# Kernel optimization log

Hardware: AMD Instinct MI355X
Metric: run time of the kernel (lower is better)

The kernel has to match this reference:

```python
import jax, jax.numpy as jnp
import numpy as np

T, N, F_IN, H, C, E = 64, 2000, 32, 64, 10, 32000
EPS = 1e-5  # BatchNorm eps (PyG BatchNorm default)


def setup_inputs() -> dict:
    key = jax.random.key(0)
    ks = jax.random.split(key, 32)
    nrm = lambda i, shape, s=0.05: jax.random.normal(ks[i], shape, jnp.float32) * s
    return {
        "x_seq": jax.random.normal(ks[0], (T, N, F_IN), jnp.float32),
        "edge_index": jax.random.randint(ks[1], (2, E), 0, N),
        "edge_weight": jax.random.uniform(ks[2], (E,), jnp.float32),
        "causal_weight": nrm(3, (N, N), 0.01),  # torch.randn(N,N)*0.01
        "lin_in_w": nrm(4, (H, F_IN)), "lin_in_b": nrm(5, (H,)),
        "fusion_w": nrm(6, (H, 2 * H)), "fusion_b": nrm(7, (H,)),
        "gcn_w0": nrm(8, (H, H)), "gcn_b0": nrm(9, (H,)),
        "gcn_w1": nrm(10, (H, H)), "gcn_b1": nrm(11, (H,)),
        "bn0_g": jnp.ones((H,), jnp.float32), "bn0_b": jnp.zeros((H,), jnp.float32),
        "bn0_m": nrm(12, (H,)), "bn0_v": 0.5 + jax.random.uniform(ks[13], (H,), jnp.float32),
        "bn1_g": jnp.ones((H,), jnp.float32), "bn1_b": jnp.zeros((H,), jnp.float32),
        "bn1_m": nrm(14, (H,)), "bn1_v": 0.5 + jax.random.uniform(ks[15], (H,), jnp.float32),
        "gru_wih0": nrm(16, (3 * H, H)), "gru_whh0": nrm(17, (3 * H, H)),
        "gru_bih0": nrm(18, (3 * H,)), "gru_bhh0": nrm(19, (3 * H,)),
        "gru_wih1": nrm(20, (3 * H, H)), "gru_whh1": nrm(21, (3 * H, H)),
        "gru_bih1": nrm(22, (3 * H,)), "gru_bhh1": nrm(23, (3 * H,)),
        "bnout_g": jnp.ones((H,), jnp.float32), "bnout_b": jnp.zeros((H,), jnp.float32),
        "bnout_m": nrm(24, (H,)), "bnout_v": 0.5 + jax.random.uniform(ks[25], (H,), jnp.float32),
        "lin_out_w": nrm(26, (C, H)), "lin_out_b": nrm(27, (C,)),
    }


def _bn(x, g, b, m, v):
    # eval-mode BatchNorm over the feature (last) axis with running stats
    return (x - m) * jax.lax.rsqrt(v + EPS) * g + b


def _gru_layer(xs, wih, whh, bih, bhh):
    # torch nn.GRU single layer, batch_first=False: xs [T, B, H_in]
    n_batch, h = xs.shape[1], whh.shape[1]

    def step(hprev, xt):
        gi = xt @ wih.T + bih            # [B, 3H]
        gh = hprev @ whh.T + bhh         # [B, 3H]
        i_r, i_z, i_n = jnp.split(gi, 3, axis=-1)
        h_r, h_z, h_n = jnp.split(gh, 3, axis=-1)
        r = jax.nn.sigmoid(i_r + h_r)
        z = jax.nn.sigmoid(i_z + h_z)
        n = jnp.tanh(i_n + r * h_n)
        hnew = (1.0 - z) * n + z * hprev
        return hnew, hnew

    h0 = jnp.zeros((n_batch, h), xs.dtype)
    _, ys = jax.lax.scan(step, h0, xs)
    return ys


def reference(x_seq, edge_index, edge_weight, causal_weight, lin_in_w, lin_in_b,
              fusion_w, fusion_b, gcn_w0, gcn_b0, gcn_w1, gcn_b1,
              bn0_g, bn0_b, bn0_m, bn0_v, bn1_g, bn1_b, bn1_m, bn1_v,
              gru_wih0, gru_whh0, gru_bih0, gru_bhh0,
              gru_wih1, gru_whh1, gru_bih1, gru_bhh1,
              bnout_g, bnout_b, bnout_m, bnout_v, lin_out_w, lin_out_b):
    n = x_seq.shape[1]
    src, dst = edge_index[0], edge_index[1]
    loops = jnp.arange(n)
    # GCN normalization with added self-loops (PyG gcn_norm, fill_value=1)
    src_f = jnp.concatenate([src, loops])
    dst_f = jnp.concatenate([dst, loops])
    w_f = jnp.concatenate([edge_weight, jnp.ones((n,), edge_weight.dtype)])
    deg = jnp.zeros((n,), x_seq.dtype).at[dst_f].add(w_f)
    dis = jax.lax.rsqrt(jnp.maximum(deg, 1e-12))
    norm = dis[src_f] * w_f * dis[dst_f]             # [E+N]

    # per-timestep pipeline, vectorized over T (same math as the Python loop)
    x = jax.nn.relu(jnp.einsum('tnf,hf->tnh', x_seq, lin_in_w) + lin_in_b)  # [T,N,H]
    wc = jax.nn.softmax(causal_weight, axis=1)                              # [N,N]
    x_agg = jnp.einsum('ij,tjh->tih', wc, x)
    x = jax.nn.relu(jnp.concatenate([x, x_agg], axis=-1) @ fusion_w.T + fusion_b)

    def gcn(xx, w, b):
        xw = xx @ w.T                                         # [T,N,H]
        msgs = jnp.take(xw, src_f, axis=1) * norm[None, :, None]  # [T,E+N,H]
        agg = jnp.zeros_like(xw).at[:, dst_f].add(msgs)
        return agg + b

    x = jax.nn.relu(_bn(gcn(x, gcn_w0, gcn_b0), bn0_g, bn0_b, bn0_m, bn0_v))
    # dropout between GCN layers is identity in eval mode
    x = jax.nn.relu(_bn(gcn(x, gcn_w1, gcn_b1), bn1_g, bn1_b, bn1_m, bn1_v))

    h = _gru_layer(x, gru_wih0, gru_whh0, gru_bih0, gru_bhh0)
    h = _gru_layer(h, gru_wih1, gru_whh1, gru_bih1, gru_bhh1)
    h_last = jax.nn.relu(_bn(h[-1], bnout_g, bnout_b, bnout_m, bnout_v))
    out = h_last @ lin_out_w.T + lin_out_b                   # [N, C]
    return jax.nn.log_softmax(out, axis=-1)
```

## Files before the change

### kernel.cpp

```cpp
#include <hip/hip_runtime.h>
#include <hip/hip_bf16.h>
#include <math.h>

#define TT 64
#define NN 2000
#define FIN 32
#define HH 64
#define CC 10
#define EE 32000
#define ETOT 34000
#define THL 4096
#define EPSBN 1e-5f
#define NB 16

#define OFF_WC   0u
#define OFF_XA   4000000u
#define OFF_XB   12192000u
#define OFF_XC   20384000u
#define OFF_DEG  28576000u
#define OFF_H1   28578048u
#define OFF_CNT  28706048u
#define OFF_CUR  28708096u
#define OFF_OFF  28710144u
#define OFF_CSRS 28712208u
#define OFF_CSRN 28746224u
#define OFF_HST  28780240u

typedef __attribute__((ext_vector_type(8))) short short8v;
typedef __attribute__((ext_vector_type(4))) float f32x4;

__device__ __forceinline__ float fsigmoid(float x) { return 1.f / (1.f + __expf(-x)); }
__device__ __forceinline__ float ftanh(float x) {
    float e = __expf(2.f * x);
    return (e - 1.f) / (e + 1.f);
}
__device__ __forceinline__ unsigned short f2bf(float f) {
    __hip_bfloat16 h = __float2bfloat16(f);
    return *reinterpret_cast<unsigned short*>(&h);
}
__device__ __forceinline__ float bf2f(unsigned short u) {
    unsigned int x = ((unsigned int)u) << 16;
    return __int_as_float(x);
}
__device__ __forceinline__ void gload_lds16(const unsigned short* g, unsigned short* l) {
    __builtin_amdgcn_global_load_lds(
        (const __attribute__((address_space(1))) unsigned int*)g,
        (__attribute__((address_space(3))) unsigned int*)l,
        16, 0, 0);
}

__global__ void k_zero(int* cnt, int* cur, float* deg) {
    int i = blockIdx.x * 256 + threadIdx.x;
    if (i < 2048) { cnt[i] = 0; cur[i] = 0; deg[i] = 0.f; }
}

__global__ void k_count(const int* __restrict__ ei, const float* __restrict__ ew,
                        int* cnt, float* deg) {
    int e = blockIdx.x * 256 + threadIdx.x;
    if (e < ETOT) {
        int dst; float w;
        if (e < EE) { dst = ei[EE + e]; w = ew[e]; }
        else        { dst = e - EE;     w = 1.f; }
        atomicAdd(&cnt[dst], 1);
        atomicAdd(&deg[dst], w);
    }
}

__global__ __launch_bounds__(1024) void k_scan(const int* __restrict__ cnt, int* off) {
    __shared__ int s[2048];
    int tid = threadIdx.x;
    s[tid]        = (tid        < NN) ? cnt[tid]        : 0;
    s[tid + 1024] = (tid + 1024 < NN) ? cnt[tid + 1024] : 0;
    __syncthreads();
    for (int d = 1; d < 2048; d <<= 1) {
        int idx = (tid + 1) * (d << 1) - 1;
        if (idx < 2048) s[idx] += s[idx - d];
        __syncthreads();
    }
    if (tid == 0) s[2047] = 0;
    __syncthreads();
    for (int d = 1024; d >= 1; d >>= 1) {
        int idx = (tid + 1) * (d << 1) - 1;
        if (idx < 2048) { int t = s[idx - d]; s[idx - d] = s[idx]; s[idx] += t; }
        __syncthreads();
    }
    off[tid] = s[tid];
    off[tid + 1024] = s[tid + 1024];
}

__global__ void k_fill(const int* __restrict__ ei, const float* __restrict__ ew,
                       const float* __restrict__ deg, const int* __restrict__ off,
                       int* cur, int* csr_src, float* csr_nrm) {
    int e = blockIdx.x * 256 + threadIdx.x;
    if (e < ETOT) {
        int src, dst; float w;
        if (e < EE) { src = ei[e]; dst = ei[EE + e]; w = ew[e]; }
        else        { src = dst = e - EE;            w = 1.f; }
        float ds = rsqrtf(fmaxf(deg[src], 1e-12f));
        float dd = rsqrtf(fmaxf(deg[dst], 1e-12f));
        int pos = off[dst] + atomicAdd(&cur[dst], 1);
        csr_src[pos] = src;
        csr_nrm[pos] = ds * w * dd;
    }
}

__global__ __launch_bounds__(256) void k_softmax(const float* __restrict__ CW,
                                                 unsigned short* __restrict__ WCH) {
    __shared__ float row[NN];
    __shared__ float red[256];
    int r = blockIdx.x, tid = threadIdx.x;
    const float* in = CW + (size_t)r * NN;
    float mx = -1e30f;
    for (int i = tid; i < NN; i += 256) { float v = in[i]; row[i] = v; mx = fmaxf(mx, v); }
    red[tid] = mx; __syncthreads();
    for (int s = 128; s > 0; s >>= 1) {
        if (tid < s) red[tid] = fmaxf(red[tid], red[tid + s]);
        __syncthreads();
    }
    mx = red[0]; __syncthreads();
    float sm = 0.f;
    for (int i = tid; i < NN; i += 256) { float e = __expf(row[i] - mx); row[i] = e; sm += e; }
    red[tid] = sm; __syncthreads();
    for (int s = 128; s > 0; s >>= 1) {
        if (tid < s) red[tid] += red[tid + s];
        __syncthreads();
    }
    float inv = 1.f / red[0];
    unsigned short* out = WCH + (size_t)r * 2048;
    for (int i = tid; i < 2048; i += 256)
        out[i] = (i < NN) ? f2bf(row[i] * inv) : (unsigned short)0;
}

__global__ __launch_bounds__(256) void k_lin2(const float* __restrict__ XS,
                                              const float* __restrict__ W,
                                              const float* __restrict__ b,
                                              float* __restrict__ OUT) {
    __shared__ float Wt[FIN][68];
    __shared__ float As[FIN][68];
    int tid = threadIdx.x;
    int n = blockIdx.x;
    for (int i = tid; i < HH * FIN; i += 256) { int o = i >> 5, k = i & 31; Wt[k][o] = W[i]; }
    int row = tid >> 2, kq = tid & 3;
    {
        const float4* src = (const float4*)(XS + ((size_t)row * NN + n) * FIN + kq * 8);
        float4 v0 = src[0], v1 = src[1];
        As[kq * 8 + 0][row] = v0.x; As[kq * 8 + 1][row] = v0.y;
        As[kq * 8 + 2][row] = v0.z; As[kq * 8 + 3][row] = v0.w;
        As[kq * 8 + 4][row] = v1.x; As[kq * 8 + 5][row] = v1.y;
        As[kq * 8 + 6][row] = v1.z; As[kq * 8 + 7][row] = v1.w;
    }
    __syncthreads();
    int tx = tid & 15, ty = tid >> 4;
    float acc[4][4] = {};
#pragma unroll
    for (int k = 0; k < FIN; ++k) {
        float4 av = *(const float4*)&As[k][ty * 4];
        float4 wv = *(const float4*)&Wt[k][tx * 4];
        acc[0][0] += av.x * wv.x; acc[0][1] += av.x * wv.y; acc[0][2] += av.x * wv.z; acc[0][3] += av.x * wv.w;
        acc[1][0] += av.y * wv.x; acc[1][1] += av.y * wv.y; acc[1][2] += av.y * wv.z; acc[1][3] += av.y * wv.w;
        acc[2][0] += av.z * wv.x; acc[2][1] += av.z * wv.y; acc[2][2] += av.z * wv.z; acc[2][3] += av.z * wv.w;
        acc[3][0] += av.w * wv.x; acc[3][1] += av.w * wv.y; acc[3][2] += av.w * wv.z; acc[3][3] += av.w * wv.w;
    }
    float4 bv = *(const float4*)(b + tx * 4);
#pragma unroll
    for (int ii = 0; ii < 4; ++ii) {
        float4 o;
        o.x = fmaxf(acc[ii][0] + bv.x, 0.f);
        o.y = fmaxf(acc[ii][1] + bv.y, 0.f);
        o.z = fmaxf(acc[ii][2] + bv.z, 0.f);
        o.w = fmaxf(acc[ii][3] + bv.w, 0.f);
        *(float4*)(OUT + ((size_t)n * TT + ty * 4 + ii) * HH + tx * 4) = o;
    }
}

__global__ __launch_bounds__(256) void k_tr(const float* __restrict__ X,
                                            unsigned short* __restrict__ XT) {
    __shared__ unsigned short tile[64][65];
    int cb = blockIdx.x * 64;
    int kb = blockIdx.y * 64;
    int tid = threadIdx.x;
    int r = tid >> 2, cq = tid & 3;
    const float4* src = (const float4*)(X + (size_t)(kb + r) * THL + cb + cq * 16);
#pragma unroll
    for (int j = 0; j < 4; ++j) {
        float4 v = src[j];
        tile[cq * 16 + j * 4 + 0][r] = f2bf(v.x);
        tile[cq * 16 + j * 4 + 1][r] = f2bf(v.y);
        tile[cq * 16 + j * 4 + 2][r] = f2bf(v.z);
        tile[cq * 16 + j * 4 + 3][r] = f2bf(v.w);
    }
    __syncthreads();
    int cl = tid >> 2, kq = tid & 3;
    unsigned short tmp[16];
#pragma unroll
    for (int j = 0; j < 16; ++j) tmp[j] = tile[cl][kq * 16 + j];
    unsigned short* dst = XT + (size_t)(cb + cl) * 2048 + kb + kq * 16;
    *(uint4*)dst = *(uint4*)tmp;
    *(uint4*)(dst + 8) = *(uint4*)(tmp + 8);
}

__global__ __launch_bounds__(256, 1) void k_gemm_bf(const unsigned short* __restrict__ A,
                                                    const unsigned short* __restrict__ B,
                                                    unsigned short* __restrict__ CH) {
    __shared__ unsigned short As[128][64];
    __shared__ unsigned short Bs[128][64];
    int tid = threadIdx.x;
    int mb = blockIdx.y * 128, nb = blockIdx.x * 128;
    int w = tid >> 6, lane = tid & 63;
    int wr = w >> 1, wc = w & 1;
    int l15 = lane & 15, l4 = lane >> 4;
    f32x4 acc[4][4] = {};
    int r_base = w * 8 + (lane >> 3);
    int colu = (lane & 7) * 8;
    for (int kt = 0; kt < 32; ++kt) {
        __syncthreads();
#pragma unroll
        for (int c = 0; c < 4; ++c) {
            int row = c * 32 + r_base;
            gload_lds16(A + (size_t)(mb + row) * 2048 + kt * 64 + colu, &As[c * 32 + w * 8][0]);
            gload_lds16(B + (size_t)(nb + row) * 2048 + kt * 64 + colu, &Bs[c * 32 + w * 8][0]);
        }
        __syncthreads();
#pragma unroll
        for (int kk = 0; kk < 2; ++kk) {
            short8v af[4], bfr[4];
#pragma unroll
            for (int f = 0; f < 4; ++f) {
                af[f]  = *(const short8v*)&As[wr * 64 + f * 16 + l15][kk * 32 + l4 * 8];
                bfr[f] = *(const short8v*)&Bs[wc * 64 + f * 16 + l15][kk * 32 + l4 * 8];
            }
#pragma unroll
            for (int fm = 0; fm < 4; ++fm)
#pragma unroll
                for (int fn = 0; fn < 4; ++fn)
                    acc[fm][fn] = __builtin_amdgcn_mfma_f32_16x16x32_bf16(af[fm], bfr[fn], acc[fm][fn], 0, 0, 0);
        }
    }
    unsigned short* epi = (unsigned short*)(&As[0][0]) + (size_t)w * (16 * 72);
    int erow8 = lane >> 3;
    int ecol8 = lane & 7;
#pragma unroll
    for (int fm = 0; fm < 4; ++fm) {
        __syncthreads();
#pragma unroll
        for (int fn = 0; fn < 4; ++fn)
#pragma unroll
            for (int rr = 0; rr < 4; ++rr)
                epi[(l4 * 4 + rr) * 72 + fn * 16 + l15] = f2bf(acc[fm][fn][rr]);
        __syncthreads();
#pragma unroll
        for (int rh = 0; rh < 2; ++rh) {
            int lrow = rh * 8 + erow8;
            int grow = mb + wr * 64 + fm * 16 + lrow;
            if (grow < NN) {
                *(uint4*)(CH + (size_t)grow * THL + nb + wc * 64 + ecol8 * 8)
                    = *(const uint4*)&epi[lrow * 72 + ecol8 * 8];
            }
        }
    }
}

__global__ __launch_bounds__(256) void k_fus2(const float* __restrict__ X,
                                              const unsigned short* __restrict__ XAH,
                                              const float* __restrict__ W,
                                              const float* __restrict__ b,
                                              float* __restrict__ OUT) {
    __shared__ float Wt[2 * HH][68];
    __shared__ float As[HH][68];
    int tid = threadIdx.x;
    size_t r0 = (size_t)blockIdx.x * 64;
    for (int i = tid; i < HH * 2 * HH; i += 256) { int o = i >> 7, k = i & 127; Wt[k][o] = W[i]; }
    int row = tid >> 2, kq = tid & 3;
    int tx = tid & 15, ty = tid >> 4;
    float acc[4][4] = {};
    __syncthreads();
    {
        const float4* src = (const float4*)(X + (r0 + row) * HH + kq * 16);
#pragma unroll
        for (int j = 0; j < 4; ++j) {
            float4 v = src[j];
            As[kq * 16 + j * 4 + 0][row] = v.x;
            As[kq * 16 + j * 4 + 1][row] = v.y;
            As[kq * 16 + j * 4 + 2][row] = v.z;
            As[kq * 16 + j * 4 + 3][row] = v.w;
        }
    }
    __syncthreads();
#pragma unroll
    for (int k = 0; k < HH; ++k) {
        float4 av = *(const float4*)&As[k][ty * 4];
        float4 wv = *(const float4*)&Wt[k][tx * 4];
        acc[0][0] += av.x * wv.x; acc[0][1] += av.x * wv.y; acc[0][2] += av.x * wv.z; acc[0][3] += av.x * wv.w;
        acc[1][0] += av.y * wv.x; acc[1][1] += av.y * wv.y; acc[1][2] += av.y * wv.z; acc[1][3] += av.y * wv.w;
        acc[2][0] += av.z * wv.x; acc[2][1] += av.z * wv.y; acc[2][2] += av.z * wv.z; acc[2][3] += av.z * wv.w;
        acc[3][0] += av.w * wv.x; acc[3][1] += av.w * wv.y; acc[3][2] += av.w * wv.z; acc[3][3] += av.w * wv.w;
    }
    __syncthreads();
    {
        const uint4* s = (const uint4*)(XAH + (r0 + row) * HH + kq * 16);
        uint4 u0 = s[0], u1 = s[1];
        unsigned short us[16];
        *(uint4*)us = u0; *(uint4*)(us + 8) = u1;
#pragma unroll
        for (int j = 0; j < 16; ++j)
            As[kq * 16 + j][row] = bf2f(us[j]);
    }
    __syncthreads();
#pragma unroll
    for (int k = 0; k < HH; ++k) {
        float4 av = *(const float4*)&As[k][ty * 4];
        float4 wv = *(const float4*)&Wt[HH + k][tx * 4];
        acc[0][0] += av.x * wv.x; acc[0][1] += av.x * wv.y; acc[0][2] += av.x * wv.z; acc[0][3] += av.x * wv.w;
        acc[1][0] += av.y * wv.x; acc[1][1] += av.y * wv.y; acc[1][2] += av.y * wv.z; acc[1][3] += av.y * wv.w;
        acc[2][0] += av.z * wv.x; acc[2][1] += av.z * wv.y; acc[2][2] += av.z * wv.z; acc[2][3] += av.z * wv.w;
        acc[3][0] += av.w * wv.x; acc[3][1] += av.w * wv.y; acc[3][2] += av.w * wv.z; acc[3][3] += av.w * wv.w;
    }
    float4 bv = *(const float4*)(b + tx * 4);
#pragma unroll
    for (int ii = 0; ii < 4; ++ii) {
        float4 o;
        o.x = fmaxf(acc[ii][0] + bv.x, 0.f);
        o.y = fmaxf(acc[ii][1] + bv.y, 0.f);
        o.z = fmaxf(acc[ii][2] + bv.z, 0.f);
        o.w = fmaxf(acc[ii][3] + bv.w, 0.f);
        *(float4*)(OUT + (r0 + ty * 4 + ii) * HH + tx * 4) = o;
    }
}

__global__ __launch_bounds__(256) void k_xw2(const float* __restrict__ IN,
                                             const float* __restrict__ W,
                                             unsigned short* __restrict__ OUT) {
    __shared__ float Wt[HH][68];
    __shared__ float As[HH][68];
    int tid = threadIdx.x;
    size_t r0 = (size_t)blockIdx.x * 64;
    for (int i = tid; i < HH * HH; i += 256) { int o = i >> 6, k = i & 63; Wt[k][o] = W[i]; }
    int row = tid >> 2, kq = tid & 3;
    {
        const float4* src = (const float4*)(IN + (r0 + row) * HH + kq * 16);
#pragma unroll
        for (int j = 0; j < 4; ++j) {
            float4 v = src[j];
            As[kq * 16 + j * 4 + 0][row] = v.x;
            As[kq * 16 + j * 4 + 1][row] = v.y;
            As[kq * 16 + j * 4 + 2][row] = v.z;
            As[kq * 16 + j * 4 + 3][row] = v.w;
        }
    }
    __syncthreads();
    int tx = tid & 15, ty = tid >> 4;
    float acc[4][4] = {};
#pragma unroll
    for (int k = 0; k < HH; ++k) {
        float4 av = *(const float4*)&As[k][ty * 4];
        float4 wv = *(const float4*)&Wt[k][tx * 4];
        acc[0][0] += av.x * wv.x; acc[0][1] += av.x * wv.y; acc[0][2] += av.x * wv.z; acc[0][3] += av.x * wv.w;
        acc[1][0] += av.y * wv.x; acc[1][1] += av.y * wv.y; acc[1][2] += av.y * wv.z; acc[1][3] += av.y * wv.w;
        acc[2][0] += av.z * wv.x; acc[2][1] += av.z * wv.y; acc[2][2] += av.z * wv.z; acc[2][3] += av.z * wv.w;
        acc[3][0] += av.w * wv.x; acc[3][1] += av.w * wv.y; acc[3][2] += av.w * wv.z; acc[3][3] += av.w * wv.w;
    }
#pragma unroll
    for (int ii = 0; ii < 4; ++ii) {
        unsigned int p0 = (unsigned int)f2bf(acc[ii][0]) | ((unsigned int)f2bf(acc[ii][1]) << 16);
        unsigned int p1 = (unsigned int)f2bf(acc[ii][2]) | ((unsigned int)f2bf(acc[ii][3]) << 16);
        uint2 pk; pk.x = p0; pk.y = p1;
        *(uint2*)(OUT + (r0 + ty * 4 + ii) * HH + tx * 4) = pk;
    }
}

__global__ __launch_bounds__(256) void k_agg(const unsigned short* __restrict__ XW,
                                             const int* __restrict__ off,
                                             const int* __restrict__ csr_src,
                                             const float* __restrict__ csr_nrm,
                                             const float* __restrict__ bias,
                                             const float* __restrict__ g,
                                             const float* __restrict__ bb,
                                             const float* __restrict__ m,
                                             const float* __restrict__ v,
                                             float* __restrict__ OUT) {
    int dst = blockIdx.x, ch = blockIdx.y, tid = threadIdx.x;
    int base = ch * 1024 + tid * 4;
    float4 acc = make_float4(0.f, 0.f, 0.f, 0.f);
    int beg = off[dst], end = off[dst + 1];
    for (int e = beg; e < end; ++e) {
        int src = csr_src[e];
        float w = csr_nrm[e];
        uint2 u = *(const uint2*)(XW + (size_t)src * THL + base);
        acc.x += w * bf2f((unsigned short)(u.x & 0xffff));
        acc.y += w * bf2f((unsigned short)(u.x >> 16));
        acc.z += w * bf2f((unsigned short)(u.y & 0xffff));
        acc.w += w * bf2f((unsigned short)(u.y >> 16));
    }
    int h0 = base & 63;
    float4 bs = *(const float4*)(bias + h0);
    float4 gv = *(const float4*)(g + h0);
    float4 vv = *(const float4*)(v + h0);
    float4 mv = *(const float4*)(m + h0);
    float4 bv = *(const float4*)(bb + h0);
    float4 o;
    o.x = fmaxf((acc.x + bs.x - mv.x) * rsqrtf(vv.x + EPSBN) * gv.x + bv.x, 0.f);
    o.y = fmaxf((acc.y + bs.y - mv.y) * rsqrtf(vv.y + EPSBN) * gv.y + bv.y, 0.f);
    o.z = fmaxf((acc.z + bs.z - mv.z) * rsqrtf(vv.z + EPSBN) * gv.z + bv.z, 0.f);
    o.w = fmaxf((acc.w + bs.w - mv.w) * rsqrtf(vv.w + EPSBN) * gv.w + bv.w, 0.f);
    *(float4*)(OUT + (size_t)dst * THL + base) = o;
}

__global__ __launch_bounds__(256, 1) void k_gruM(const float* __restrict__ IN,
                                                 const float* __restrict__ wih0, const float* __restrict__ whh0,
                                                 const float* __restrict__ bih0, const float* __restrict__ bhh0,
                                                 const float* __restrict__ wih1, const float* __restrict__ whh1,
                                                 const float* __restrict__ bih1, const float* __restrict__ bhh1,
                                                 float* __restrict__ hout) {
    __shared__ float hf0[NB][68];
    __shared__ float hf1[NB][68];
    __shared__ unsigned short hb0[NB][72];
    __shared__ unsigned short hb1[NB][72];
    int tid = threadIdx.x;
    int w = tid >> 6, lane = tid & 63;
    int l15 = lane & 15, l4 = lane >> 4;
    int nb0 = blockIdx.x * NB;
    short8v bw[4][3][2];
    const float* Wm[4] = { wih0, whh0, wih1, whh1 };
#pragma unroll
    for (int m = 0; m < 4; ++m)
#pragma unroll
        for (int g = 0; g < 3; ++g)
#pragma unroll
            for (int kk = 0; kk < 2; ++kk) {
                const float* src = Wm[m] + (size_t)(64 * g + 16 * w + l15) * HH + kk * 32 + l4 * 8;
                float4 v0 = *(const float4*)src;
                float4 v1 = *(const float4*)(src + 4);
                short8v f;
                f[0] = (short)f2bf(v0.x); f[1] = (short)f2bf(v0.y);
                f[2] = (short)f2bf(v0.z); f[3] = (short)f2bf(v0.w);
                f[4] = (short)f2bf(v1.x); f[5] = (short)f2bf(v1.y);
                f[6] = (short)f2bf(v1.z); f[7] = (short)f2bf(v1.w);
                bw[m][g][kk] = f;
            }
    int jr = 16 * w + l15;
    float b0r = bih0[jr] + bhh0[jr];
    float b0z = bih0[64 + jr] + bhh0[64 + jr];
    float b0n = bih0[128 + jr];
    float h0n = bhh0[128 + jr];
    float b1r = bih1[jr] + bhh1[jr];
    float b1z = bih1[64 + jr] + bhh1[64 + jr];
    float b1n = bih1[128 + jr];
    float h1n = bhh1[128 + jr];
    for (int i = tid; i < NB * 68; i += 256) { ((float*)hf0)[i] = 0.f; ((float*)hf1)[i] = 0.f; }
    for (int i = tid; i < NB * 72; i += 256) { ((unsigned short*)hb0)[i] = 0; ((unsigned short*)hb1)[i] = 0; }
    __syncthreads();
    const float* xb = IN + (size_t)(nb0 + l15) * (TT * HH);
    float4 xv[4];
    {
        const float* xs = xb + 0 * HH + l4 * 8;
        xv[0] = *(const float4*)xs; xv[1] = *(const float4*)(xs + 4);
        const float* xs2 = xb + 0 * HH + 32 + l4 * 8;
        xv[2] = *(const float4*)xs2; xv[3] = *(const float4*)(xs2 + 4);
    }
#pragma unroll 1
    for (int t = 0; t <= TT; ++t) {
        bool act0 = (t < TT);
        bool act1 = (t >= 1);
        short8v ax[2], ah0[2], ah1[2];
#pragma unroll
        for (int kk = 0; kk < 2; ++kk) {
            float4 v0 = xv[kk * 2], v1 = xv[kk * 2 + 1];
            short8v f;
            f[0] = (short)f2bf(v0.x); f[1] = (short)f2bf(v0.y);
            f[2] = (short)f2bf(v0.z); f[3] = (short)f2bf(v0.w);
            f[4] = (short)f2bf(v1.x); f[5] = (short)f2bf(v1.y);
            f[6] = (short)f2bf(v1.z); f[7] = (short)f2bf(v1.w);
            ax[kk] = f;
            ah0[kk] = *(const short8v*)&hb0[l15][kk * 32 + l4 * 8];
            ah1[kk] = *(const short8v*)&hb1[l15][kk * 32 + l4 * 8];
        }
        __syncthreads();
        if (t + 1 < TT) {
            const float* xs = xb + (size_t)(t + 1) * HH + l4 * 8;
            xv[0] = *(const float4*)xs; xv[1] = *(const float4*)(xs + 4);
            const float* xs2 = xb + (size_t)(t + 1) * HH + 32 + l4 * 8;
            xv[2] = *(const float4*)xs2; xv[3] = *(const float4*)(xs2 + 4);
        }
        if (act0) {
            f32x4 gr = { b0r, b0r, b0r, b0r };
            f32x4 gz = { b0z, b0z, b0z, b0z };
            f32x4 gn = { b0n, b0n, b0n, b0n };
            f32x4 hr = { 0.f, 0.f, 0.f, 0.f };
            f32x4 hz = { 0.f, 0.f, 0.f, 0.f };
            f32x4 hn = { h0n, h0n, h0n, h0n };
#pragma unroll
            for (int kk = 0; kk < 2; ++kk) {
                gr = __builtin_amdgcn_mfma_f32_16x16x32_bf16(ax[kk], bw[0][0][kk], gr, 0, 0, 0);
                gz = __builtin_amdgcn_mfma_f32_16x16x32_bf16(ax[kk], bw[0][1][kk], gz, 0, 0, 0);
                gn = __builtin_amdgcn_mfma_f32_16x16x32_bf16(ax[kk], bw[0][2][kk], gn, 0, 0, 0);
                hr = __builtin_amdgcn_mfma_f32_16x16x32_bf16(ah0[kk], bw[1][0][kk], hr, 0, 0, 0);
                hz = __builtin_amdgcn_mfma_f32_16x16x32_bf16(ah0[kk], bw[1][1][kk], hz, 0, 0, 0);
                hn = __builtin_amdgcn_mfma_f32_16x16x32_bf16(ah0[kk], bw[1][2][kk], hn, 0, 0, 0);
            }
#pragma unroll
            for (int i = 0; i < 4; ++i) {
                int node = l4 * 4 + i;
                float r = fsigmoid(gr[i] + hr[i]);
                float z = fsigmoid(gz[i] + hz[i]);
                float nn2 = ftanh(gn[i] + r * hn[i]);
                float ho = hf0[node][jr];
                float hv = (1.f - z) * nn2 + z * ho;
                hf0[node][jr] = hv;
                hb0[node][jr] = f2bf(hv);
            }
        }
        if (act1) {
            f32x4 gr = { b1r, b1r, b1r, b1r };
            f32x4 gz = { b1z, b1z, b1z, b1z };
            f32x4 gn = { b1n, b1n, b1n, b1n };
            f32x4 hr = { 0.f, 0.f, 0.f, 0.f };
            f32x4 hz = { 0.f, 0.f, 0.f, 0.f };
            f32x4 hn = { h1n, h1n, h1n, h1n };
#pragma unroll
            for (int kk = 0; kk < 2; ++kk) {
                gr = __builtin_amdgcn_mfma_f32_16x16x32_bf16(ah0[kk], bw[2][0][kk], gr, 0, 0, 0);
                gz = __builtin_amdgcn_mfma_f32_16x16x32_bf16(ah0[kk], bw[2][1][kk], gz, 0, 0, 0);
                gn = __builtin_amdgcn_mfma_f32_16x16x32_bf16(ah0[kk], bw[2][2][kk], gn, 0, 0, 0);
                hr = __builtin_amdgcn_mfma_f32_16x16x32_bf16(ah1[kk], bw[3][0][kk], hr, 0, 0, 0);
                hz = __builtin_amdgcn_mfma_f32_16x16x32_bf16(ah1[kk], bw[3][1][kk], hz, 0, 0, 0);
                hn = __builtin_amdgcn_mfma_f32_16x16x32_bf16(ah1[kk], bw[3][2][kk], hn, 0, 0, 0);
            }
#pragma unroll
            for (int i = 0; i < 4; ++i) {
                int node = l4 * 4 + i;
                float r = fsigmoid(gr[i] + hr[i]);
                float z = fsigmoid(gz[i] + hz[i]);
                float nn2 = ftanh(gn[i] + r * hn[i]);
                float ho = hf1[node][jr];
                float hv = (1.f - z) * nn2 + z * ho;
                hf1[node][jr] = hv;
                hb1[node][jr] = f2bf(hv);
            }
        }
        __syncthreads();
    }
    for (int i = tid; i < NB * HH; i += 256) {
        int node = i >> 6, j = i & 63;
        hout[(size_t)(nb0 + node) * HH + j] = hf1[node][j];
    }
}

__global__ __launch_bounds__(256) void k_head(const float* __restrict__ Hf,
                                              const float* __restrict__ g, const float* __restrict__ b,
                                              const float* __restrict__ m, const float* __restrict__ v,
                                              const float* __restrict__ W, const float* __restrict__ wb,
                                              float* __restrict__ out) {
    __shared__ float hb[4][HH];
    __shared__ float lg[4][CC];
    int tid = threadIdx.x;
    int n0 = blockIdx.x * 4;
    int wv = tid >> 6, lane = tid & 63;
    int n = n0 + wv;
    float x = Hf[(size_t)n * HH + lane];
    x = (x - m[lane]) * rsqrtf(v[lane] + EPSBN) * g[lane] + b[lane];
    hb[wv][lane] = fmaxf(x, 0.f);
    __syncthreads();
    if (tid < 4 * CC) {
        int nn = tid / CC, c = tid % CC;
        float acc = wb[c];
        for (int f = 0; f < HH; ++f) acc += hb[nn][f] * W[c * HH + f];
        lg[nn][c] = acc;
    }
    __syncthreads();
    if (tid < 4 * CC) {
        int nn = tid / CC, c = tid % CC;
        float mx = -1e30f;
#pragma unroll
        for (int i = 0; i < CC; ++i) mx = fmaxf(mx, lg[nn][i]);
        float s = 0.f;
#pragma unroll
        for (int i = 0; i < CC; ++i) s += __expf(lg[nn][i] - mx);
        out[(size_t)(n0 + nn) * CC + c] = lg[nn][c] - mx - __logf(s);
    }
}

extern "C" void kernel_launch(void* const* d_in, const int* in_sizes, int n_in,
                              void* d_out, int out_size, void* d_ws, size_t ws_size,
                              hipStream_t stream) {
    const float* x_seq     = (const float*)d_in[0];
    const int*   edge_idx  = (const int*)d_in[1];
    const float* edge_w    = (const float*)d_in[2];
    const float* causal_w  = (const float*)d_in[3];
    const float* lin_in_w  = (const float*)d_in[4];
    const float* lin_in_b  = (const float*)d_in[5];
    const float* fusion_w  = (const float*)d_in[6];
    const float* fusion_b  = (const float*)d_in[7];
    const float* gcn_w0    = (const float*)d_in[8];
    const float* gcn_b0    = (const float*)d_in[9];
    const float* gcn_w1    = (const float*)d_in[10];
    const float* gcn_b1    = (const float*)d_in[11];
    const float* bn0_g = (const float*)d_in[12], *bn0_b = (const float*)d_in[13];
    const float* bn0_m = (const float*)d_in[14], *bn0_v = (const float*)d_in[15];
    const float* bn1_g = (const float*)d_in[16], *bn1_b = (const float*)d_in[17];
    const float* bn1_m = (const float*)d_in[18], *bn1_v = (const float*)d_in[19];
    const float* wih0 = (const float*)d_in[20], *whh0 = (const float*)d_in[21];
    const float* bih0 = (const float*)d_in[22], *bhh0 = (const float*)d_in[23];
    const float* wih1 = (const float*)d_in[24], *whh1 = (const float*)d_in[25];
    const float* bih1 = (const float*)d_in[26], *bhh1 = (const float*)d_in[27];
    const float* bno_g = (const float*)d_in[28], *bno_b = (const float*)d_in[29];
    const float* bno_m = (const float*)d_in[30], *bno_v = (const float*)d_in[31];
    const float* lout_w = (const float*)d_in[32], *lout_b = (const float*)d_in[33];
    float* out = (float*)d_out;

    float* wsf = (float*)d_ws;
    unsigned short* WCH = (unsigned short*)(wsf + OFF_WC);
    float* XA  = wsf + OFF_XA;
    float* XB  = wsf + OFF_XB;
    float* XC  = wsf + OFF_XC;
    unsigned short* XAT = (unsigned short*)(wsf + OFF_XC);
    unsigned short* XBH = (unsigned short*)(wsf + OFF_XB);
    float* DEG = wsf + OFF_DEG;
    int* CNT   = (int*)(wsf + OFF_CNT);
    int* CUR   = (int*)(wsf + OFF_CUR);
    int* OFFP  = (int*)(wsf + OFF_OFF);
    int* CSRS  = (int*)(wsf + OFF_CSRS);
    float* CSRN = wsf + OFF_CSRN;
    float* HST  = wsf + OFF_HST;

    k_zero<<<8, 256, 0, stream>>>(CNT, CUR, DEG);
    k_count<<<(ETOT + 255) / 256, 256, 0, stream>>>(edge_idx, edge_w, CNT, DEG);
    k_scan<<<1, 1024, 0, stream>>>(CNT, OFFP);
    k_fill<<<(ETOT + 255) / 256, 256, 0, stream>>>(edge_idx, edge_w, DEG, OFFP, CUR, CSRS, CSRN);

    hipMemsetAsync(WCH, 0, (size_t)2048 * 2048 * 2, stream);
    k_softmax<<<NN, 256, 0, stream>>>(causal_w, WCH);
    k_lin2<<<NN, 256, 0, stream>>>(x_seq, lin_in_w, lin_in_b, XA);
    dim3 tg(THL / 64, 2048 / 64);
    k_tr<<<tg, 256, 0, stream>>>(XA, XAT);
    dim3 gg(THL / 128, 2048 / 128);
    k_gemm_bf<<<gg, 256, 0, stream>>>(WCH, XAT, XBH);
    k_fus2<<<NN, 256, 0, stream>>>(XA, XBH, fusion_w, fusion_b, XC);
    k_xw2<<<NN, 256, 0, stream>>>(XC, gcn_w0, XBH);
    dim3 ag(NN, 4);
    k_agg<<<ag, 256, 0, stream>>>(XBH, OFFP, CSRS, CSRN, gcn_b0, bn0_g, bn0_b, bn0_m, bn0_v, XA);
    k_xw2<<<NN, 256, 0, stream>>>(XA, gcn_w1, XBH);
    k_agg<<<ag, 256, 0, stream>>>(XBH, OFFP, CSRS, CSRN, gcn_b1, bn1_g, bn1_b, bn1_m, bn1_v, XC);

    k_gruM<<<NN / NB, 256, 0, stream>>>(XC, wih0, whh0, bih0, bhh0,
                                        wih1, whh1, bih1, bhh1, HST);

    k_head<<<NN / 4, 256, 0, stream>>>(HST, bno_g, bno_b, bno_m, bno_v, lout_w, lout_b, out);
}
```

Measured before the change: 362.0 us.

## Fuse GCN weight projections into fusion-linear and first aggregation kernels

The fusion-linear kernel now keeps its ReLU output in shared memory and multiplies it by gcn_w0 in the same block, writing bf16 XW directly. The first aggregation kernel applies bias, BatchNorm and ReLU, then multiplies each block's 16 rows by gcn_w1 in shared memory to produce the second layer's XW. This removes two kernel launches and two fp32 intermediate round trips through global memory. In exchange, every aggregation block reloads the 64x64 weight matrix, and the fusion kernel writes its output in place over its own input rows.

```diff
diff --git a/kernel.cpp b/kernel.cpp
--- a/kernel.cpp
+++ b/kernel.cpp
@@ -260,11 +260,12 @@
     }
 }
 
-__global__ __launch_bounds__(256) void k_fus2(const float* __restrict__ X,
-                                              const unsigned short* __restrict__ XAH,
-                                              const float* __restrict__ W,
-                                              const float* __restrict__ b,
-                                              float* __restrict__ OUT) {
+__global__ __launch_bounds__(256) void k_fusxw(const float* __restrict__ X,
+                                               const unsigned short* __restrict__ XAH,
+                                               const float* __restrict__ W,
+                                               const float* __restrict__ b,
+                                               const float* __restrict__ W0,
+                                               unsigned short* __restrict__ OUT) {
     __shared__ float Wt[2 * HH][68];
     __shared__ float As[HH][68];
     int tid = threadIdx.x;
@@ -316,56 +317,87 @@
         acc[3][0] += av.w * wv.x; acc[3][1] += av.w * wv.y; acc[3][2] += av.w * wv.z; acc[3][3] += av.w * wv.w;
     }
     float4 bv = *(const float4*)(b + tx * 4);
+    __syncthreads();
 #pragma unroll
     for (int ii = 0; ii < 4; ++ii) {
-        float4 o;
-        o.x = fmaxf(acc[ii][0] + bv.x, 0.f);
-        o.y = fmaxf(acc[ii][1] + bv.y, 0.f);
-        o.z = fmaxf(acc[ii][2] + bv.z, 0.f);
-        o.w = fmaxf(acc[ii][3] + bv.w, 0.f);
-        *(float4*)(OUT + (r0 + ty * 4 + ii) * HH + tx * 4) = o;
-    }
-}
-
-__global__ __launch_bounds__(256) void k_xw2(const float* __restrict__ IN,
-                                             const float* __restrict__ W,
-                                             unsigned short* __restrict__ OUT) {
-    __shared__ float Wt[HH][68];
-    __shared__ float As[HH][68];
-    int tid = threadIdx.x;
-    size_t r0 = (size_t)blockIdx.x * 64;
-    for (int i = tid; i < HH * HH; i += 256) { int o = i >> 6, k = i & 63; Wt[k][o] = W[i]; }
-    int row = tid >> 2, kq = tid & 3;
-    {
-        const float4* src = (const float4*)(IN + (r0 + row) * HH + kq * 16);
-#pragma unroll
-        for (int j = 0; j < 4; ++j) {
-            float4 v = src[j];
-            As[kq * 16 + j * 4 + 0][row] = v.x;
-            As[kq * 16 + j * 4 + 1][row] = v.y;
-            As[kq * 16 + j * 4 + 2][row] = v.z;
-            As[kq * 16 + j * 4 + 3][row] = v.w;
-        }
-    }
-    __syncthreads();
-    int tx = tid & 15, ty = tid >> 4;
-    float acc[4][4] = {};
+        As[tx * 4 + 0][ty * 4 + ii] = fmaxf(acc[ii][0] + bv.x, 0.f);
+        As[tx * 4 + 1][ty * 4 + ii] = fmaxf(acc[ii][1] + bv.y, 0.f);
+        As[tx * 4 + 2][ty * 4 + ii] = fmaxf(acc[ii][2] + bv.z, 0.f);
+        As[tx * 4 + 3][ty * 4 + ii] = fmaxf(acc[ii][3] + bv.w, 0.f);
+    }
+    for (int i = tid; i < HH * HH; i += 256) { int o = i >> 6, k = i & 63; Wt[k][o] = W0[i]; }
+    __syncthreads();
+    float a2[4][4] = {};
 #pragma unroll
     for (int k = 0; k < HH; ++k) {
         float4 av = *(const float4*)&As[k][ty * 4];
         float4 wv = *(const float4*)&Wt[k][tx * 4];
-        acc[0][0] += av.x * wv.x; acc[0][1] += av.x * wv.y; acc[0][2] += av.x * wv.z; acc[0][3] += av.x * wv.w;
-        acc[1][0] += av.y * wv.x; acc[1][1] += av.y * wv.y; acc[1][2] += av.y * wv.z; acc[1][3] += av.y * wv.w;
-        acc[2][0] += av.z * wv.x; acc[2][1] += av.z * wv.y; acc[2][2] += av.z * wv.z; acc[2][3] += av.z * wv.w;
-        acc[3][0] += av.w * wv.x; acc[3][1] += av.w * wv.y; acc[3][2] += av.w * wv.z; acc[3][3] += av.w * wv.w;
+        a2[0][0] += av.x * wv.x; a2[0][1] += av.x * wv.y; a2[0][2] += av.x * wv.z; a2[0][3] += av.x * wv.w;
+        a2[1][0] += av.y * wv.x; a2[1][1] += av.y * wv.y; a2[1][2] += av.y * wv.z; a2[1][3] += av.y * wv.w;
+        a2[2][0] += av.z * wv.x; a2[2][1] += av.z * wv.y; a2[2][2] += av.z * wv.z; a2[2][3] += av.z * wv.w;
+        a2[3][0] += av.w * wv.x; a2[3][1] += av.w * wv.y; a2[3][2] += av.w * wv.z; a2[3][3] += av.w * wv.w;
     }
 #pragma unroll
     for (int ii = 0; ii < 4; ++ii) {
-        unsigned int p0 = (unsigned int)f2bf(acc[ii][0]) | ((unsigned int)f2bf(acc[ii][1]) << 16);
-        unsigned int p1 = (unsigned int)f2bf(acc[ii][2]) | ((unsigned int)f2bf(acc[ii][3]) << 16);
+        unsigned int p0 = (unsigned int)f2bf(a2[ii][0]) | ((unsigned int)f2bf(a2[ii][1]) << 16);
+        unsigned int p1 = (unsigned int)f2bf(a2[ii][2]) | ((unsigned int)f2bf(a2[ii][3]) << 16);
         uint2 pk; pk.x = p0; pk.y = p1;
         *(uint2*)(OUT + (r0 + ty * 4 + ii) * HH + tx * 4) = pk;
     }
+}
+
+__global__ __launch_bounds__(256) void k_aggxw(const unsigned short* __restrict__ XW,
+                                               const int* __restrict__ off,
+                                               const int* __restrict__ csr_src,
+                                               const float* __restrict__ csr_nrm,
+                                               const float* __restrict__ bias,
+                                               const float* __restrict__ g,
+                                               const float* __restrict__ bb,
+                                               const float* __restrict__ m,
+                                               const float* __restrict__ v,
+                                               const float* __restrict__ W1,
+                                               unsigned short* __restrict__ OUT) {
+    __shared__ float Rs[HH][18];
+    __shared__ float Wt[HH][68];
+    int dst = blockIdx.x, ch = blockIdx.y, tid = threadIdx.x;
+    int base = ch * 1024 + tid * 4;
+    for (int i = tid; i < HH * HH; i += 256) { int o = i >> 6, k = i & 63; Wt[k][o] = W1[i]; }
+    float4 acc = make_float4(0.f, 0.f, 0.f, 0.f);
+    int beg = off[dst], end = off[dst + 1];
+    for (int e = beg; e < end; ++e) {
+        int src = csr_src[e];
+        float w = csr_nrm[e];
+        uint2 u = *(const uint2*)(XW + (size_t)src * THL + base);
+        acc.x += w * bf2f((unsigned short)(u.x & 0xffff));
+        acc.y += w * bf2f((unsigned short)(u.x >> 16));
+        acc.z += w * bf2f((unsigned short)(u.y & 0xffff));
+        acc.w += w * bf2f((unsigned short)(u.y >> 16));
+    }
+    int h0 = base & 63;
+    int rloc = tid >> 4;
+    float4 bs = *(const float4*)(bias + h0);
+    float4 gv = *(const float4*)(g + h0);
+    float4 vv = *(const float4*)(v + h0);
+    float4 mv = *(const float4*)(m + h0);
+    float4 bv = *(const float4*)(bb + h0);
+    Rs[h0 + 0][rloc] = fmaxf((acc.x + bs.x - mv.x) * rsqrtf(vv.x + EPSBN) * gv.x + bv.x, 0.f);
+    Rs[h0 + 1][rloc] = fmaxf((acc.y + bs.y - mv.y) * rsqrtf(vv.y + EPSBN) * gv.y + bv.y, 0.f);
+    Rs[h0 + 2][rloc] = fmaxf((acc.z + bs.z - mv.z) * rsqrtf(vv.z + EPSBN) * gv.z + bv.z, 0.f);
+    Rs[h0 + 3][rloc] = fmaxf((acc.w + bs.w - mv.w) * rsqrtf(vv.w + EPSBN) * gv.w + bv.w, 0.f);
+    __syncthreads();
+    int c4 = tid & 15;
+    float a2[4] = {0.f, 0.f, 0.f, 0.f};
+#pragma unroll
+    for (int k = 0; k < HH; ++k) {
+        float a = Rs[k][rloc];
+        float4 wv = *(const float4*)&Wt[k][c4 * 4];
+        a2[0] += a * wv.x; a2[1] += a * wv.y; a2[2] += a * wv.z; a2[3] += a * wv.w;
+    }
+    size_t grow = (size_t)dst * TT + ch * 16 + rloc;
+    unsigned int p0 = (unsigned int)f2bf(a2[0]) | ((unsigned int)f2bf(a2[1]) << 16);
+    unsigned int p1 = (unsigned int)f2bf(a2[2]) | ((unsigned int)f2bf(a2[3]) << 16);
+    uint2 pk; pk.x = p0; pk.y = p1;
+    *(uint2*)(OUT + grow * HH + c4 * 4) = pk;
 }
 
 __global__ __launch_bounds__(256) void k_agg(const unsigned short* __restrict__ XW,
@@ -610,10 +642,10 @@
     float* wsf = (float*)d_ws;
     unsigned short* WCH = (unsigned short*)(wsf + OFF_WC);
     float* XA  = wsf + OFF_XA;
-    float* XB  = wsf + OFF_XB;
     float* XC  = wsf + OFF_XC;
     unsigned short* XAT = (unsigned short*)(wsf + OFF_XC);
     unsigned short* XBH = (unsigned short*)(wsf + OFF_XB);
+    unsigned short* XW1 = (unsigned short*)(wsf + OFF_XA);
     float* DEG = wsf + OFF_DEG;
     int* CNT   = (int*)(wsf + OFF_CNT);
     int* CUR   = (int*)(wsf + OFF_CUR);
@@ -634,12 +666,11 @@
     k_tr<<<tg, 256, 0, stream>>>(XA, XAT);
     dim3 gg(THL / 128, 2048 / 128);
     k_gemm_bf<<<gg, 256, 0, stream>>>(WCH, XAT, XBH);
-    k_fus2<<<NN, 256, 0, stream>>>(XA, XBH, fusion_w, fusion_b, XC);
-    k_xw2<<<NN, 256, 0, stream>>>(XC, gcn_w0, XBH);
+    k_fusxw<<<NN, 256, 0, stream>>>(XA, XBH, fusion_w, fusion_b, gcn_w0, XBH);
     dim3 ag(NN, 4);
-    k_agg<<<ag, 256, 0, stream>>>(XBH, OFFP, CSRS, CSRN, gcn_b0, bn0_g, bn0_b, bn0_m, bn0_v, XA);
-    k_xw2<<<NN, 256, 0, stream>>>(XA, gcn_w1, XBH);
-    k_agg<<<ag, 256, 0, stream>>>(XBH, OFFP, CSRS, CSRN, gcn_b1, bn1_g, bn1_b, bn1_m, bn1_v, XC);
+    k_aggxw<<<ag, 256, 0, stream>>>(XBH, OFFP, CSRS, CSRN, gcn_b0, bn0_g, bn0_b, bn0_m, bn0_v,
+                                    gcn_w1, XW1);
+    k_agg<<<ag, 256, 0, stream>>>(XW1, OFFP, CSRS, CSRN, gcn_b1, bn1_g, bn1_b, bn1_m, bn1_v, XC);
 
     k_gruM<<<NN / NB, 256, 0, stream>>>(XC, wih0, whh0, bih0, bhh0,
                                         wih1, whh1, bih1, bhh1, HST);
```

After: 359.3 us. No clear change (-0.8%).
